# Kernel tuning notes

Hardware: AMD Instinct MI355X
Metric: run time of the kernel (lower is better)

Reference implementation:

```python
import jax, jax.numpy as jnp
import numpy as np

B, T, D, L = 64, 512, 1024, 32


def setup_inputs() -> dict:
    key = jax.random.key(0)
    ks = jax.random.split(key, 6)
    x = jax.random.normal(ks[0], (B, T, D), jnp.float32)
    W = jax.random.normal(ks[1], (D, L), jnp.float32) * 0.02  # TruncatedNormal(stddev=0.02) analogue
    b = jnp.zeros((L,), jnp.float32)
    transitions = jax.random.normal(ks[2], (L, L), jnp.float32) * 0.1
    label = jax.random.randint(ks[3], (B, T), 0, L).astype(jnp.int32)
    seqlen = jax.random.randint(ks[4], (B,), 1, T + 1).astype(jnp.int32)
    mask = jnp.arange(T)[None, :] < seqlen[:, None]
    return {"x": x, "W": W, "b": b, "transitions": transitions,
            "label": label, "seqlen": seqlen, "mask": mask}


def crf_sequence_score(emissions, label, seqlen, transitions):
    # emissions: [B,T,L]
    Bc, Tc, Lc = emissions.shape
    m = (jnp.arange(Tc)[None, :] < seqlen[:, None]).astype(emissions.dtype)  # [B,T]
    unary = jnp.take_along_axis(emissions, label[..., None].astype(jnp.int32), axis=-1)[..., 0]
    unary = jnp.sum(unary * m, axis=1)
    trans = transitions[label[:, :-1], label[:, 1:]]  # [B,T-1]
    mt = (jnp.arange(1, Tc)[None, :] < seqlen[:, None]).astype(emissions.dtype)
    binary = jnp.sum(trans * mt, axis=1)
    return unary + binary


def crf_log_norm(emissions, seqlen, transitions):
    Bc, Tc, Lc = emissions.shape
    alpha0 = emissions[:, 0]  # [B,L]
    valid = (jnp.arange(1, Tc)[None, :] < seqlen[:, None]).T  # [T-1,B]
    emits = jnp.moveaxis(emissions[:, 1:], 1, 0)  # [T-1,B,L]

    def step(alpha, inp):
        emit_t, v = inp
        new = jax.nn.logsumexp(alpha[:, :, None] + transitions[None], axis=1) + emit_t
        return jnp.where(v[:, None], new, alpha), None

    alpha, _ = jax.lax.scan(step, alpha0, (emits, valid))
    return jax.nn.logsumexp(alpha, axis=-1)  # [B]


def crf_decode(emissions, transitions, seqlen):
    Bc, Tc, Lc = emissions.shape
    alpha0 = emissions[:, 0]
    idx = jnp.arange(Lc, dtype=jnp.int32)
    valid = (jnp.arange(1, Tc)[None, :] < seqlen[:, None]).T  # [T-1,B]
    emits = jnp.moveaxis(emissions[:, 1:], 1, 0)

    def fwd(alpha, inp):
        emit_t, v = inp
        scores = alpha[:, :, None] + transitions[None]  # [B,L,L]
        best = jnp.max(scores, axis=1) + emit_t
        bp = jnp.argmax(scores, axis=1).astype(jnp.int32)  # [B,L]
        alpha_new = jnp.where(v[:, None], best, alpha)
        bp = jnp.where(v[:, None], bp, idx[None, :])  # identity bp on padded steps
        return alpha_new, bp

    alpha, bps = jax.lax.scan(fwd, alpha0, (emits, valid))  # bps: [T-1,B,L]
    last = jnp.argmax(alpha, axis=-1).astype(jnp.int32)  # [B]

    def bwd(tag, bp):
        prev = jnp.take_along_axis(bp, tag[:, None], axis=1)[:, 0]
        return prev, tag

    first, tags = jax.lax.scan(bwd, last, bps, reverse=True)  # tags[i] = tag at t=i+1
    seq = jnp.concatenate([first[None], tags], axis=0)  # [T,B]
    return jnp.moveaxis(seq, 0, 1)  # [B,T]


def reference(x, W, b, transitions, label, seqlen, mask):
    emissions = jnp.einsum('btd,dl->btl', x, W) + b  # Dense projection
    ll = crf_sequence_score(emissions, label, seqlen, transitions) - crf_log_norm(emissions, seqlen, transitions)
    loss = jnp.mean(-ll)
    vit = crf_decode(emissions, transitions, seqlen)
    tp = jnp.sum(((label > 0) & (vit == label)).astype(jnp.float32))
    tn = jnp.sum(((label > 0) & (vit != label)).astype(jnp.float32))
    fp = jnp.sum((mask & (label == 0) & (vit > 0)).astype(jnp.float32))
    return loss, vit, tp, tn, fp
```

## Files before the change

### kernel.cpp

```cpp
#include <hip/hip_runtime.h>
#include <stdint.h>
#include <math.h>

#define Bn 64
#define Tn 512
#define Dn 1024
#define Ln 32
#define LOG2E 1.4426950408889634f
#define LN2f  0.6931471805599453f

#define EMIS_OFF 0
#define LOGNORM_OFF (Bn * Tn * Ln)
#define SCORE_OFF (LOGNORM_OFF + Bn)
#define CNT_OFF (SCORE_OFF + Bn)

#define MAX3(a,b,c) fmaxf(fmaxf((a),(b)),(c))

template<int K>
__device__ __forceinline__ float rorf(float v) {
    return __int_as_float(__builtin_amdgcn_update_dpp(
        0, __float_as_int(v), 0x120 | K, 0xF, 0xF, true));
}

__device__ __forceinline__ float opaque_copy(float v) {
    float r;
    asm volatile("v_mov_b32 %0, %1" : "=v"(r) : "v"(v));
    return r;
}

__device__ __forceinline__ void swap32p(float p, float& x, float& y) {
    x = p;
    y = opaque_copy(p);
    asm volatile("v_permlane32_swap_b32 %0, %1" : "+v"(x), "+v"(y));
}
__device__ __forceinline__ void swap16p(float p, float& x, float& y) {
    x = p;
    y = opaque_copy(p);
    asm volatile("v_permlane16_swap_b32 %0, %1" : "+v"(x), "+v"(y));
}

#define BM 128
#define KB 32
#define XSS 132

__global__ __launch_bounds__(256) void gemm_emis(
    const float* __restrict__ x, const float* __restrict__ Wm,
    const float* __restrict__ bias, const int* __restrict__ seqlen,
    float* __restrict__ emis)
{
    int b  = blockIdx.x >> 2;
    int t0 = (blockIdx.x & 3) * BM;
    if (t0 >= seqlen[b]) return;

    __shared__ __align__(16) float xs[KB * XSS];
    __shared__ __align__(16) float wsh[KB * Ln];

    int tid = threadIdx.x;
    int cg = tid & 7;
    int rg = tid >> 3;

    const float* xrow = x + (size_t)(b * Tn + t0) * Dn;

    float acc[4][4];
    #pragma unroll
    for (int z = 0; z < 4; z++)
        #pragma unroll
        for (int c = 0; c < 4; c++) acc[z][c] = 0.f;

    float4 xr[4]; float4 wr;
    #pragma unroll
    for (int u = 0; u < 4; u++) {
        int f = tid + 256 * u;
        xr[u] = *(const float4*)(xrow + (size_t)(f >> 3) * Dn + (f & 7) * 4);
    }
    wr = *(const float4*)(Wm + tid * 4);

    for (int k0 = 0; k0 < Dn; k0 += KB) {
        __syncthreads();
        #pragma unroll
        for (int u = 0; u < 4; u++) {
            int f = tid + 256 * u;
            int lrow = f >> 3, kk = f & 7;
            xs[(4 * kk + 0) * XSS + lrow] = xr[u].x;
            xs[(4 * kk + 1) * XSS + lrow] = xr[u].y;
            xs[(4 * kk + 2) * XSS + lrow] = xr[u].z;
            xs[(4 * kk + 3) * XSS + lrow] = xr[u].w;
        }
        *(float4*)(wsh + tid * 4) = wr;
        __syncthreads();

        int kn = k0 + KB;
        if (kn < Dn) {
            #pragma unroll
            for (int u = 0; u < 4; u++) {
                int f = tid + 256 * u;
                xr[u] = *(const float4*)(xrow + (size_t)(f >> 3) * Dn + kn + (f & 7) * 4);
            }
            wr = *(const float4*)(Wm + (size_t)kn * Ln + tid * 4);
        }

        #pragma unroll 8
        for (int k = 0; k < KB; k++) {
            float4 a = *(const float4*)(xs + k * XSS + 4 * rg);
            float4 w = *(const float4*)(wsh + k * Ln + 4 * cg);
            float av[4] = {a.x, a.y, a.z, a.w};
            float wv[4] = {w.x, w.y, w.z, w.w};
            #pragma unroll
            for (int z = 0; z < 4; z++)
                #pragma unroll
                for (int c = 0; c < 4; c++)
                    acc[z][c] = fmaf(av[z], wv[c], acc[z][c]);
        }
    }

    float4 bv = *(const float4*)(bias + 4 * cg);
    float bb[4] = {bv.x, bv.y, bv.z, bv.w};
    #pragma unroll
    for (int z = 0; z < 4; z++) {
        float4 o;
        o.x = acc[z][0] + bb[0];
        o.y = acc[z][1] + bb[1];
        o.z = acc[z][2] + bb[2];
        o.w = acc[z][3] + bb[3];
        *(float4*)(emis + (size_t)(b * Tn + t0 + 4 * rg + z) * Ln + 4 * cg) = o;
    }
}

#define CH 64

__global__ __launch_bounds__(512) void crf_forward(
    const float* __restrict__ emis, const float* __restrict__ trans,
    const int* __restrict__ label, const int* __restrict__ seqlen,
    float* __restrict__ out, float* __restrict__ wsf)
{
    __shared__ __align__(16) float es[Tn * Ln];
    __shared__ __align__(16) float al[Tn * Ln];
    __shared__ __align__(16) float trs[Ln * Ln];
    __shared__ uint8_t bp[Tn * Ln];
    __shared__ uint8_t Fm[16 * 32];
    __shared__ int btag[16];
    __shared__ int s_last;
    __shared__ float credA[8], credB[8], credC[8];

    int tid = threadIdx.x;
    int b = blockIdx.x;
    int slen = seqlen[b];
    int wv = tid >> 6;
    int lane = tid & 63;
    int j = lane & 31;

    const float* eb = emis + (size_t)b * Tn * Ln;

    {
        int n4 = slen * (Ln / 4);
        for (int i4 = tid; i4 < n4; i4 += 512)
            ((float4*)es)[i4] = ((const float4*)eb)[i4];
    }
    if (tid < 256) ((float4*)trs)[tid] = ((const float4*)trans)[tid];
    {
        uint32_t* bp32 = (uint32_t*)bp;
        for (int w = tid; w < Tn * Ln / 4; w += 512)
            bp32[w] = 0x03020100u + 0x04040404u * (uint32_t)(w & 7);
    }

    int rq[16];
    {
        float qf = (float)(lane & 15);
        rq[0]  = lane & 15;
        rq[1]  = (int)rorf<1>(qf);   rq[2]  = (int)rorf<2>(qf);
        rq[3]  = (int)rorf<3>(qf);   rq[4]  = (int)rorf<4>(qf);
        rq[5]  = (int)rorf<5>(qf);   rq[6]  = (int)rorf<6>(qf);
        rq[7]  = (int)rorf<7>(qf);   rq[8]  = (int)rorf<8>(qf);
        rq[9]  = (int)rorf<9>(qf);   rq[10] = (int)rorf<10>(qf);
        rq[11] = (int)rorf<11>(qf);  rq[12] = (int)rorf<12>(qf);
        rq[13] = (int)rorf<13>(qf);  rq[14] = (int)rorf<14>(qf);
        rq[15] = (int)rorf<15>(qf);
    }
    bool useX;
    {
        float px, py; swap16p((float)lane, px, py);
        useX = (px == (float)(lane ^ 16));
    }
    int hoff = (lane & 32) ? 16 : 0;
    int hidx = (lane & 15) + hoff;
    int row2 = (lane >> 4) & 3;
    bool keepC = (row2 == 0) || (row2 == 3);

    __syncthreads();

    float av = 0.f, emit = 0.f;
    float a = 0.f, eemit = 0.f;
    int   Eacc = 0;
    float tr[32];
    float e2[16];

    if (wv == 0) {
        #pragma unroll
        for (int k = 0; k < 16; k++) tr[k] = trs[(rq[k] + hoff) * Ln + j];
        av = es[hidx];
        al[hidx] = av;
        emit = es[Ln + j];
    } else if (wv == 1) {
        #pragma unroll
        for (int k = 0; k < 16; k++) e2[k] = exp2f(trs[(rq[k] + hoff) * Ln + j] * LOG2E);
        a = exp2f(es[hidx] * LOG2E);
        eemit = exp2f(es[Ln + j] * LOG2E);
    } else {
        #pragma unroll
        for (int i = 0; i < 32; i++) tr[i] = trs[i * Ln + j];
    }

    for (int c = 0; c < Tn / CH; c++) {
        int tb = (c == 0) ? 1 : c * CH;
        int te = (c + 1) * CH; if (te > slen) te = slen;

        if (wv == 0) {
            #pragma unroll 2
            for (int t = tb; t < te; t++) {
                int tnx = (t + 1 < slen) ? (t + 1) : (slen - 1);
                float emitn = es[tnx * Ln + j];
                float vv0  = av           + tr[0];
                float vv1  = rorf<1>(av)  + tr[1];
                float vv2  = rorf<2>(av)  + tr[2];
                float vv3  = rorf<3>(av)  + tr[3];
                float vv4  = rorf<4>(av)  + tr[4];
                float vv5  = rorf<5>(av)  + tr[5];
                float vv6  = rorf<6>(av)  + tr[6];
                float vv7  = rorf<7>(av)  + tr[7];
                float vv8  = rorf<8>(av)  + tr[8];
                float vv9  = rorf<9>(av)  + tr[9];
                float vv10 = rorf<10>(av) + tr[10];
                float vv11 = rorf<11>(av) + tr[11];
                float vv12 = rorf<12>(av) + tr[12];
                float vv13 = rorf<13>(av) + tr[13];
                float vv14 = rorf<14>(av) + tr[14];
                float vv15 = rorf<15>(av) + tr[15];
                float g0 = MAX3(vv0,  vv1,  vv2);
                float g1 = MAX3(vv3,  vv4,  vv5);
                float g2 = MAX3(vv6,  vv7,  vv8);
                float g3 = MAX3(vv9,  vv10, vv11);
                float g4 = MAX3(vv12, vv13, vv14);
                float h0 = MAX3(g0, g1, g2);
                float h1 = MAX3(g3, g4, vv15);
                float p = fmaxf(h0, h1);
                float x, y; swap32p(p, x, y);
                float cmb = fmaxf(x, y) + emit;
                al[t * Ln + j] = cmb;
                float x2, y2; swap16p(cmb, x2, y2);
                float z = useX ? x2 : y2;
                av = keepC ? cmb : z;
                emit = emitn;
            }
        } else if (wv == 1) {
            #pragma unroll 2
            for (int t = tb; t < te; t++) {
                int tnx = (t + 1 < slen) ? (t + 1) : (slen - 1);
                float emitn = es[tnx * Ln + j];
                float eemitn = exp2f(emitn * LOG2E);
                float s0 = a           * e2[0];
                float s1 = rorf<1>(a)  * e2[1];
                float s2 = rorf<2>(a)  * e2[2];
                float s3 = rorf<3>(a)  * e2[3];
                s0 = fmaf(rorf<4>(a),  e2[4],  s0);
                s1 = fmaf(rorf<5>(a),  e2[5],  s1);
                s2 = fmaf(rorf<6>(a),  e2[6],  s2);
                s3 = fmaf(rorf<7>(a),  e2[7],  s3);
                s0 = fmaf(rorf<8>(a),  e2[8],  s0);
                s1 = fmaf(rorf<9>(a),  e2[9],  s1);
                s2 = fmaf(rorf<10>(a), e2[10], s2);
                s3 = fmaf(rorf<11>(a), e2[11], s3);
                s0 = fmaf(rorf<12>(a), e2[12], s0);
                s1 = fmaf(rorf<13>(a), e2[13], s1);
                s2 = fmaf(rorf<14>(a), e2[14], s2);
                s3 = fmaf(rorf<15>(a), e2[15], s3);
                float pp = (s0 + s1) + (s2 + s3);
                float x, y; swap32p(pp, x, y);
                float s = (x + y) * eemit;
                float an;
                if ((t & 3) == 0) {
                    unsigned sb = (unsigned)__builtin_amdgcn_readfirstlane(__float_as_int(s));
                    int e = (int)((sb >> 23) & 0xFFu) - 127;
                    Eacc += e;
                    an = ldexpf(s, -e);
                } else {
                    an = s;
                }
                float x2, y2; swap16p(an, x2, y2);
                float z = useX ? x2 : y2;
                a = keepC ? an : z;
                eemit = eemitn;
            }
        } else if (c == 0) {
            if (wv == 2) {
                const int* lb = label + (size_t)b * Tn;
                float acc = 0.f;
                for (int t = lane; t < Tn; t += 64) {
                    if (t < slen) {
                        int lc = lb[t];
                        acc += es[t * Ln + lc];
                        if (t >= 1) acc += trs[lb[t - 1] * Ln + lc];
                    }
                }
                #pragma unroll
                for (int off = 32; off >= 1; off >>= 1) acc += __shfl_xor(acc, off);
                if (lane == 0) wsf[SCORE_OFF + b] = acc;
            }
        } else {
            int stripe = (wv - 2) * 2 + (lane >> 5);
            int pb = ((c - 1) == 0) ? 1 : (c - 1) * CH;
            int pe = c * CH; if (pe > slen) pe = slen;
            for (int t = pb + stripe; t < pe; t += 12) {
                const float* ar = al + (t - 1) * Ln;
                float vv[32];
                #pragma unroll
                for (int i = 0; i < 32; i += 4) {
                    float4 a4 = *(const float4*)(ar + i);
                    vv[i]     = a4.x + tr[i];
                    vv[i + 1] = a4.y + tr[i + 1];
                    vv[i + 2] = a4.z + tr[i + 2];
                    vv[i + 3] = a4.w + tr[i + 3];
                }
                float mv[16]; int mi[16];
                #pragma unroll
                for (int i = 0; i < 16; i++) {
                    bool g = vv[2*i+1] > vv[2*i];
                    mv[i] = g ? vv[2*i+1] : vv[2*i];
                    mi[i] = g ? (2*i+1) : (2*i);
                }
                #pragma unroll
                for (int i = 0; i < 8; i++) {
                    bool g = mv[2*i+1] > mv[2*i];
                    mv[i] = g ? mv[2*i+1] : mv[2*i];
                    mi[i] = g ? mi[2*i+1] : mi[2*i];
                }
                #pragma unroll
                for (int i = 0; i < 4; i++) {
                    bool g = mv[2*i+1] > mv[2*i];
                    mv[i] = g ? mv[2*i+1] : mv[2*i];
                    mi[i] = g ? mi[2*i+1] : mi[2*i];
                }
                #pragma unroll
                for (int i = 0; i < 2; i++) {
                    bool g = mv[2*i+1] > mv[2*i];
                    mv[i] = g ? mv[2*i+1] : mv[2*i];
                    mi[i] = g ? mi[2*i+1] : mi[2*i];
                }
                bp[t * Ln + j] = (uint8_t)mi[0];
            }
        }
        __syncthreads();
    }

    if (wv == 0) {
        float mm = av; int ai = hidx;
        #pragma unroll
        for (int off = 32; off >= 1; off >>= 1) {
            float om = __shfl_xor(mm, off);
            int   oi = __shfl_xor(ai, off);
            if (om > mm || (om == mm && oi < ai)) { mm = om; ai = oi; }
        }
        if (lane == 0) s_last = ai;
    } else if (wv == 1) {
        float ss = a;
        #pragma unroll
        for (int off = 32; off >= 1; off >>= 1) ss += __shfl_xor(ss, off);
        if (lane == 0)
            wsf[LOGNORM_OFF + b] = (log2f(ss) - 1.0f + (float)Eacc) * LN2f;
    } else {
        int stripe = (wv - 2) * 2 + (lane >> 5);
        int cc = Tn / CH - 1;
        int pb = cc * CH;
        int pe = Tn; if (pe > slen) pe = slen;
        for (int t = pb + stripe; t < pe; t += 12) {
            const float* ar = al + (t - 1) * Ln;
            float vv[32];
            #pragma unroll
            for (int i = 0; i < 32; i += 4) {
                float4 a4 = *(const float4*)(ar + i);
                vv[i]     = a4.x + tr[i];
                vv[i + 1] = a4.y + tr[i + 1];
                vv[i + 2] = a4.z + tr[i + 2];
                vv[i + 3] = a4.w + tr[i + 3];
            }
            float mv[16]; int mi[16];
            #pragma unroll
            for (int i = 0; i < 16; i++) {
                bool g = vv[2*i+1] > vv[2*i];
                mv[i] = g ? vv[2*i+1] : vv[2*i];
                mi[i] = g ? (2*i+1) : (2*i);
            }
            #pragma unroll
            for (int i = 0; i < 8; i++) {
                bool g = mv[2*i+1] > mv[2*i];
                mv[i] = g ? mv[2*i+1] : mv[2*i];
                mi[i] = g ? mi[2*i+1] : mi[2*i];
            }
            #pragma unroll
            for (int i = 0; i < 4; i++) {
                bool g = mv[2*i+1] > mv[2*i];
                mv[i] = g ? mv[2*i+1] : mv[2*i];
                mi[i] = g ? mi[2*i+1] : mi[2*i];
            }
            #pragma unroll
            for (int i = 0; i < 2; i++) {
                bool g = mv[2*i+1] > mv[2*i];
                mv[i] = g ? mv[2*i+1] : mv[2*i];
                mi[i] = g ? mi[2*i+1] : mi[2*i];
            }
            bp[t * Ln + j] = (uint8_t)mi[0];
        }
    }
    __syncthreads();

    int sseg = tid >> 5, ent = tid & 31;
    {
        int y = ent;
        for (int p = 32 * sseg + 31; p >= 32 * sseg; p--) y = bp[p * Ln + y];
        Fm[sseg * 32 + ent] = (uint8_t)y;
    }
    __syncthreads();
    if (tid == 0) {
        int y = s_last;
        btag[15] = y;
        for (int ss = 15; ss >= 1; ss--) { y = Fm[ss * 32 + y]; btag[ss - 1] = y; }
    }
    __syncthreads();
    int q = tid;
    int y = btag[sseg];
    for (int p = 32 * sseg + 31; p >= q + 1; p--) y = bp[p * Ln + y];
    out[1 + (size_t)b * Tn + q] = (float)y;

    int lbl = label[(size_t)b * Tn + q];
    float tpf = (lbl > 0 && y == lbl) ? 1.f : 0.f;
    float tnf = (lbl > 0 && y != lbl) ? 1.f : 0.f;
    float fpf = (q < slen && lbl == 0 && y > 0) ? 1.f : 0.f;
    #pragma unroll
    for (int off = 32; off >= 1; off >>= 1) {
        tpf += __shfl_xor(tpf, off);
        tnf += __shfl_xor(tnf, off);
        fpf += __shfl_xor(fpf, off);
    }
    if (lane == 0) { credA[wv] = tpf; credB[wv] = tnf; credC[wv] = fpf; }
    __syncthreads();
    if (tid == 0) {
        float aa = 0.f, bb2 = 0.f, cc2 = 0.f;
        #pragma unroll
        for (int w = 0; w < 8; w++) { aa += credA[w]; bb2 += credB[w]; cc2 += credC[w]; }
        wsf[CNT_OFF + b] = aa;
        wsf[CNT_OFF + Bn + b] = bb2;
        wsf[CNT_OFF + 2 * Bn + b] = cc2;
    }
}

__global__ __launch_bounds__(64) void crf_final(const float* __restrict__ wsf,
                                                float* __restrict__ out)
{
    int lane = threadIdx.x;
    float nll = wsf[LOGNORM_OFF + lane] - wsf[SCORE_OFF + lane];
    float tp = wsf[CNT_OFF + lane];
    float tn = wsf[CNT_OFF + Bn + lane];
    float fp = wsf[CNT_OFF + 2 * Bn + lane];
    #pragma unroll
    for (int off = 32; off >= 1; off >>= 1) {
        nll += __shfl_xor(nll, off);
        tp  += __shfl_xor(tp, off);
        tn  += __shfl_xor(tn, off);
        fp  += __shfl_xor(fp, off);
    }
    if (lane == 0) {
        out[0] = nll * (1.f / 64.f);
        out[1 + Bn * Tn + 0] = tp;
        out[1 + Bn * Tn + 1] = tn;
        out[1 + Bn * Tn + 2] = fp;
    }
}

extern "C" void kernel_launch(void* const* d_in, const int* in_sizes, int n_in,
                              void* d_out, int out_size, void* d_ws, size_t ws_size,
                              hipStream_t stream) {
    const float* x     = (const float*)d_in[0];
    const float* W     = (const float*)d_in[1];
    const float* bias  = (const float*)d_in[2];
    const float* trans = (const float*)d_in[3];
    const int* label   = (const int*)d_in[4];
    const int* seqlen  = (const int*)d_in[5];
    float* out = (float*)d_out;
    float* wsf = (float*)d_ws;

    gemm_emis<<<dim3(Bn * (Tn / BM)), dim3(256), 0, stream>>>(x, W, bias, seqlen, wsf + EMIS_OFF);
    crf_forward<<<dim3(Bn), dim3(512), 0, stream>>>(wsf + EMIS_OFF, trans, label, seqlen, out, wsf);
    crf_final<<<dim3(1), dim3(64), 0, stream>>>(wsf, out);
}
```

Before: 286.3 us.

## Alternate lane layouts across timesteps to drop per-step permlane16 swap in CRF recurrences

The Viterbi and log-sum-exp recurrences previously did a permlane32 reduction and then a permlane16 swap with a select on every step, just to put alpha back into the layout the next step expects. Now even and odd steps use two transition tables precomputed for two lane mappings. Each step reduces with either permlane16 or permlane32 and feeds its result straight into the next step, which removes one cross-lane swap and a select from the serial critical path. The emission prefetch is moved two steps ahead, and the asm volatile qualifiers are dropped so the compiler can schedule the swaps. The cost is twice as many transition registers and more complex index bookkeeping at the final argmax and for odd start steps.

```diff
diff --git a/kernel.cpp b/kernel.cpp
--- a/kernel.cpp
+++ b/kernel.cpp
@@ -24,19 +24,19 @@
 
 __device__ __forceinline__ float opaque_copy(float v) {
     float r;
-    asm volatile("v_mov_b32 %0, %1" : "=v"(r) : "v"(v));
+    asm("v_mov_b32 %0, %1" : "=v"(r) : "v"(v));
     return r;
 }
 
 __device__ __forceinline__ void swap32p(float p, float& x, float& y) {
     x = p;
     y = opaque_copy(p);
-    asm volatile("v_permlane32_swap_b32 %0, %1" : "+v"(x), "+v"(y));
+    asm("v_permlane32_swap_b32 %0, %1" : "+v"(x), "+v"(y));
 }
 __device__ __forceinline__ void swap16p(float p, float& x, float& y) {
     x = p;
     y = opaque_copy(p);
-    asm volatile("v_permlane16_swap_b32 %0, %1" : "+v"(x), "+v"(y));
+    asm("v_permlane16_swap_b32 %0, %1" : "+v"(x), "+v"(y));
 }
 
 #define BM 128
@@ -127,6 +127,76 @@
 }
 
 #define CH 64
+
+#define VIT_BODY(T, TRARR, SWAPFN, OE)                                       \
+  {                                                                          \
+    int tnx2 = ((T) + 2 < slen) ? ((T) + 2) : (slen - 1);                    \
+    float e2n = es[tnx2 * Ln + (OE)];                                        \
+    float vv0  = av            + TRARR[0];                                   \
+    float vv1  = rorf<1>(av)   + TRARR[1];                                   \
+    float vv2  = rorf<2>(av)   + TRARR[2];                                   \
+    float vv3  = rorf<3>(av)   + TRARR[3];                                   \
+    float vv4  = rorf<4>(av)   + TRARR[4];                                   \
+    float vv5  = rorf<5>(av)   + TRARR[5];                                   \
+    float vv6  = rorf<6>(av)   + TRARR[6];                                   \
+    float vv7  = rorf<7>(av)   + TRARR[7];                                   \
+    float vv8  = rorf<8>(av)   + TRARR[8];                                   \
+    float vv9  = rorf<9>(av)   + TRARR[9];                                   \
+    float vv10 = rorf<10>(av)  + TRARR[10];                                  \
+    float vv11 = rorf<11>(av)  + TRARR[11];                                  \
+    float vv12 = rorf<12>(av)  + TRARR[12];                                  \
+    float vv13 = rorf<13>(av)  + TRARR[13];                                  \
+    float vv14 = rorf<14>(av)  + TRARR[14];                                  \
+    float vv15 = rorf<15>(av)  + TRARR[15];                                  \
+    float g0 = MAX3(vv0,  vv1,  vv2);                                        \
+    float g1 = MAX3(vv3,  vv4,  vv5);                                        \
+    float g2 = MAX3(vv6,  vv7,  vv8);                                        \
+    float g3 = MAX3(vv9,  vv10, vv11);                                       \
+    float g4 = MAX3(vv12, vv13, vv14);                                       \
+    float h0 = MAX3(g0, g1, g2);                                             \
+    float h1 = MAX3(g3, g4, vv15);                                           \
+    float p = fmaxf(h0, h1);                                                 \
+    float xx, yy; SWAPFN(p, xx, yy);                                         \
+    float cmb = fmaxf(xx, yy) + emit;                                        \
+    al[(T) * Ln + (OE)] = cmb;                                               \
+    av = cmb;                                                                \
+    emit = emitn; emitn = e2n;                                               \
+  }
+
+#define LSE_BODY(T, EARR, SWAPFN, OE, DORENORM)                              \
+  {                                                                          \
+    int tnx2 = ((T) + 2 < slen) ? ((T) + 2) : (slen - 1);                    \
+    float rawn = es[tnx2 * Ln + (OE)];                                       \
+    float een = exp2f(rawnext * LOG2E);                                      \
+    float s0 = a           * EARR[0];                                        \
+    float s1 = rorf<1>(a)  * EARR[1];                                        \
+    float s2 = rorf<2>(a)  * EARR[2];                                        \
+    float s3 = rorf<3>(a)  * EARR[3];                                        \
+    s0 = fmaf(rorf<4>(a),  EARR[4],  s0);                                    \
+    s1 = fmaf(rorf<5>(a),  EARR[5],  s1);                                    \
+    s2 = fmaf(rorf<6>(a),  EARR[6],  s2);                                    \
+    s3 = fmaf(rorf<7>(a),  EARR[7],  s3);                                    \
+    s0 = fmaf(rorf<8>(a),  EARR[8],  s0);                                    \
+    s1 = fmaf(rorf<9>(a),  EARR[9],  s1);                                    \
+    s2 = fmaf(rorf<10>(a), EARR[10], s2);                                    \
+    s3 = fmaf(rorf<11>(a), EARR[11], s3);                                    \
+    s0 = fmaf(rorf<12>(a), EARR[12], s0);                                    \
+    s1 = fmaf(rorf<13>(a), EARR[13], s1);                                    \
+    s2 = fmaf(rorf<14>(a), EARR[14], s2);                                    \
+    s3 = fmaf(rorf<15>(a), EARR[15], s3);                                    \
+    float pp = (s0 + s1) + (s2 + s3);                                        \
+    float xx, yy; SWAPFN(pp, xx, yy);                                        \
+    float s = (xx + yy) * eemit;                                             \
+    if ((DORENORM) && (((T) & 3) == 0)) {                                    \
+        unsigned sb = (unsigned)__builtin_amdgcn_readfirstlane(__float_as_int(s)); \
+        int e = (int)((sb >> 23) & 0xFFu) - 127;                             \
+        Eacc += e;                                                           \
+        a = ldexpf(s, -e);                                                   \
+    } else {                                                                 \
+        a = s;                                                               \
+    }                                                                        \
+    eemit = een; rawnext = rawn;                                             \
+  }
 
 __global__ __launch_bounds__(512) void crf_forward(
     const float* __restrict__ emis, const float* __restrict__ trans,
@@ -176,38 +246,46 @@
         rq[13] = (int)rorf<13>(qf);  rq[14] = (int)rorf<14>(qf);
         rq[15] = (int)rorf<15>(qf);
     }
-    bool useX;
-    {
-        float px, py; swap16p((float)lane, px, py);
-        useX = (px == (float)(lane ^ 16));
-    }
-    int hoff = (lane & 32) ? 16 : 0;
-    int hidx = (lane & 15) + hoff;
-    int row2 = (lane >> 4) & 3;
-    bool keepC = (row2 == 0) || (row2 == 3);
+    int q4  = lane & 15;
+    int sb4 = (lane & 16) ? 16 : 0;
+    int sb5 = (lane & 32) ? 16 : 0;
+    int o4  = q4 + sb4;
+    int o5  = q4 + sb5;
 
     __syncthreads();
 
-    float av = 0.f, emit = 0.f;
-    float a = 0.f, eemit = 0.f;
+    float av = 0.f, emit = 0.f, emitn = 0.f;
+    float a = 0.f, eemit = 0.f, rawnext = 0.f;
     int   Eacc = 0;
-    float tr[32];
-    float e2[16];
+    float trA[16], trB[16];
+    float e2A[16], e2B[16];
+    float trH[32];
+
+    int i1 = (1 < slen) ? 1 : (slen - 1);
+    int i2 = (2 < slen) ? 2 : (slen - 1);
 
     if (wv == 0) {
         #pragma unroll
-        for (int k = 0; k < 16; k++) tr[k] = trs[(rq[k] + hoff) * Ln + j];
-        av = es[hidx];
-        al[hidx] = av;
-        emit = es[Ln + j];
+        for (int k = 0; k < 16; k++) {
+            trA[k] = trs[(rq[k] + sb5) * Ln + o4];
+            trB[k] = trs[(rq[k] + sb4) * Ln + o5];
+        }
+        av = es[o5];
+        al[o5] = av;
+        emit  = es[i1 * Ln + o4];
+        emitn = es[i2 * Ln + o5];
     } else if (wv == 1) {
         #pragma unroll
-        for (int k = 0; k < 16; k++) e2[k] = exp2f(trs[(rq[k] + hoff) * Ln + j] * LOG2E);
-        a = exp2f(es[hidx] * LOG2E);
-        eemit = exp2f(es[Ln + j] * LOG2E);
+        for (int k = 0; k < 16; k++) {
+            e2A[k] = exp2f(trs[(rq[k] + sb5) * Ln + o4] * LOG2E);
+            e2B[k] = exp2f(trs[(rq[k] + sb4) * Ln + o5] * LOG2E);
+        }
+        a = exp2f(es[o5] * LOG2E);
+        eemit   = exp2f(es[i1 * Ln + o4] * LOG2E);
+        rawnext = es[i2 * Ln + o5];
     } else {
         #pragma unroll
-        for (int i = 0; i < 32; i++) tr[i] = trs[i * Ln + j];
+        for (int i = 0; i < 32; i++) trH[i] = trs[i * Ln + j];
     }
 
     for (int c = 0; c < Tn / CH; c++) {
@@ -215,81 +293,21 @@
         int te = (c + 1) * CH; if (te > slen) te = slen;
 
         if (wv == 0) {
-            #pragma unroll 2
-            for (int t = tb; t < te; t++) {
-                int tnx = (t + 1 < slen) ? (t + 1) : (slen - 1);
-                float emitn = es[tnx * Ln + j];
-                float vv0  = av           + tr[0];
-                float vv1  = rorf<1>(av)  + tr[1];
-                float vv2  = rorf<2>(av)  + tr[2];
-                float vv3  = rorf<3>(av)  + tr[3];
-                float vv4  = rorf<4>(av)  + tr[4];
-                float vv5  = rorf<5>(av)  + tr[5];
-                float vv6  = rorf<6>(av)  + tr[6];
-                float vv7  = rorf<7>(av)  + tr[7];
-                float vv8  = rorf<8>(av)  + tr[8];
-                float vv9  = rorf<9>(av)  + tr[9];
-                float vv10 = rorf<10>(av) + tr[10];
-                float vv11 = rorf<11>(av) + tr[11];
-                float vv12 = rorf<12>(av) + tr[12];
-                float vv13 = rorf<13>(av) + tr[13];
-                float vv14 = rorf<14>(av) + tr[14];
-                float vv15 = rorf<15>(av) + tr[15];
-                float g0 = MAX3(vv0,  vv1,  vv2);
-                float g1 = MAX3(vv3,  vv4,  vv5);
-                float g2 = MAX3(vv6,  vv7,  vv8);
-                float g3 = MAX3(vv9,  vv10, vv11);
-                float g4 = MAX3(vv12, vv13, vv14);
-                float h0 = MAX3(g0, g1, g2);
-                float h1 = MAX3(g3, g4, vv15);
-                float p = fmaxf(h0, h1);
-                float x, y; swap32p(p, x, y);
-                float cmb = fmaxf(x, y) + emit;
-                al[t * Ln + j] = cmb;
-                float x2, y2; swap16p(cmb, x2, y2);
-                float z = useX ? x2 : y2;
-                av = keepC ? cmb : z;
-                emit = emitn;
-            }
+            int t = tb;
+            if ((t & 1) && t < te) { VIT_BODY(t, trA, swap32p, o4); t++; }
+            for (; t + 1 < te; t += 2) {
+                VIT_BODY(t,     trB, swap16p, o5);
+                VIT_BODY(t + 1, trA, swap32p, o4);
+            }
+            if (t < te) { VIT_BODY(t, trB, swap16p, o5); }
         } else if (wv == 1) {
-            #pragma unroll 2
-            for (int t = tb; t < te; t++) {
-                int tnx = (t + 1 < slen) ? (t + 1) : (slen - 1);
-                float emitn = es[tnx * Ln + j];
-                float eemitn = exp2f(emitn * LOG2E);
-                float s0 = a           * e2[0];
-                float s1 = rorf<1>(a)  * e2[1];
-                float s2 = rorf<2>(a)  * e2[2];
-                float s3 = rorf<3>(a)  * e2[3];
-                s0 = fmaf(rorf<4>(a),  e2[4],  s0);
-                s1 = fmaf(rorf<5>(a),  e2[5],  s1);
-                s2 = fmaf(rorf<6>(a),  e2[6],  s2);
-                s3 = fmaf(rorf<7>(a),  e2[7],  s3);
-                s0 = fmaf(rorf<8>(a),  e2[8],  s0);
-                s1 = fmaf(rorf<9>(a),  e2[9],  s1);
-                s2 = fmaf(rorf<10>(a), e2[10], s2);
-                s3 = fmaf(rorf<11>(a), e2[11], s3);
-                s0 = fmaf(rorf<12>(a), e2[12], s0);
-                s1 = fmaf(rorf<13>(a), e2[13], s1);
-                s2 = fmaf(rorf<14>(a), e2[14], s2);
-                s3 = fmaf(rorf<15>(a), e2[15], s3);
-                float pp = (s0 + s1) + (s2 + s3);
-                float x, y; swap32p(pp, x, y);
-                float s = (x + y) * eemit;
-                float an;
-                if ((t & 3) == 0) {
-                    unsigned sb = (unsigned)__builtin_amdgcn_readfirstlane(__float_as_int(s));
-                    int e = (int)((sb >> 23) & 0xFFu) - 127;
-                    Eacc += e;
-                    an = ldexpf(s, -e);
-                } else {
-                    an = s;
-                }
-                float x2, y2; swap16p(an, x2, y2);
-                float z = useX ? x2 : y2;
-                a = keepC ? an : z;
-                eemit = eemitn;
-            }
+            int t = tb;
+            if ((t & 1) && t < te) { LSE_BODY(t, e2A, swap32p, o4, 0); t++; }
+            for (; t + 1 < te; t += 2) {
+                LSE_BODY(t,     e2B, swap16p, o5, 1);
+                LSE_BODY(t + 1, e2A, swap32p, o4, 0);
+            }
+            if (t < te) { LSE_BODY(t, e2B, swap16p, o5, 1); }
         } else if (c == 0) {
             if (wv == 2) {
                 const int* lb = label + (size_t)b * Tn;
@@ -315,10 +333,10 @@
                 #pragma unroll
                 for (int i = 0; i < 32; i += 4) {
                     float4 a4 = *(const float4*)(ar + i);
-                    vv[i]     = a4.x + tr[i];
-                    vv[i + 1] = a4.y + tr[i + 1];
-                    vv[i + 2] = a4.z + tr[i + 2];
-                    vv[i + 3] = a4.w + tr[i + 3];
+                    vv[i]     = a4.x + trH[i];
+                    vv[i + 1] = a4.y + trH[i + 1];
+                    vv[i + 2] = a4.z + trH[i + 2];
+                    vv[i + 3] = a4.w + trH[i + 3];
                 }
                 float mv[16]; int mi[16];
                 #pragma unroll
@@ -352,7 +370,8 @@
     }
 
     if (wv == 0) {
-        float mm = av; int ai = hidx;
+        int oT = ((slen - 1) & 1) ? o4 : o5;
+        float mm = av; int ai = oT;
         #pragma unroll
         for (int off = 32; off >= 1; off >>= 1) {
             float om = __shfl_xor(mm, off);
@@ -377,10 +396,10 @@
             #pragma unroll
             for (int i = 0; i < 32; i += 4) {
                 float4 a4 = *(const float4*)(ar + i);
-                vv[i]     = a4.x + tr[i];
-                vv[i + 1] = a4.y + tr[i + 1];
-                vv[i + 2] = a4.z + tr[i + 2];
-                vv[i + 3] = a4.w + tr[i + 3];
+                vv[i]     = a4.x + trH[i];
+                vv[i + 1] = a4.y + trH[i + 1];
+                vv[i + 2] = a4.z + trH[i + 2];
+                vv[i + 3] = a4.w + trH[i + 3];
             }
             float mv[16]; int mi[16];
             #pragma unroll
```

New measurement: 271.7 us. 5.1% less time.
